# Kernel tuning notes

Hardware: AMD Instinct MI355X
Metric: run time of the kernel (lower is better)

The kernel has to match this reference:

```python
import jax, jax.numpy as jnp
import numpy as np

N_NODES = 50000
N_EDGES = 400000
DIM = 64
HEADS = 4
BN_EPS = 1e-5


def glorot(key, shape, fan_in, fan_out):
    std = np.sqrt(6.0 / (fan_in + fan_out))
    return jax.random.uniform(key, shape, jnp.float32, -std, std)


def setup_inputs() -> dict:
    key = jax.random.key(0)
    ks = jax.random.split(key, 6)
    x = jax.random.normal(ks[0], (N_NODES, DIM), jnp.float32)
    edge_attr = jax.random.normal(ks[1], (N_EDGES, DIM), jnp.float32)
    edge_index = jax.random.randint(ks[2], (2, N_EDGES), 0, N_NODES, jnp.int64)
    W = glorot(ks[3], (2 * DIM, HEADS * DIM), 2 * DIM, HEADS * DIM)
    att = glorot(ks[4], (1, HEADS, 2 * DIM), 2 * DIM, 1)
    bias = jnp.zeros((DIM,), jnp.float32)
    bn_gamma = jnp.ones((HEADS,), jnp.float32)
    bn_beta = jnp.zeros((HEADS,), jnp.float32)
    return {"x": x, "edge_attr": edge_attr, "W": W, "att": att,
            "bias": bias, "bn_gamma": bn_gamma, "bn_beta": bn_beta,
            "edge_index": edge_index}


def segment_softmax(a, seg, num_segments):
    # numerically stable softmax over variable-size neighborhoods (per segment)
    m = jax.ops.segment_max(a, seg, num_segments=num_segments)
    e = jnp.exp(a - m[seg])
    s = jax.ops.segment_sum(e, seg, num_segments=num_segments)
    return e / (s[seg] + 1e-16)


def reference(x, edge_attr, W, att, bias, bn_gamma, bn_beta, edge_index):
    act = jax.nn.softplus
    i, j = edge_index[0], edge_index[1]  # flow='target_to_source': i indexes x_i and aggregation
    x_i = x[i]                           # [E, D]
    x_j = x[j]                           # [E, D]
    out_i = act(jnp.concatenate([x_i, edge_attr], -1) @ W).reshape(-1, HEADS, DIM)
    out_j = act(jnp.concatenate([x_j, edge_attr], -1) @ W).reshape(-1, HEADS, DIM)
    # attention logits: [E, H]
    alpha = act((jnp.concatenate([out_i, out_j], -1) * att).sum(-1))
    # BatchNorm1d over heads with batch statistics (biased variance)
    mu = alpha.mean(0)
    var = alpha.var(0)
    alpha = (alpha - mu) * jax.lax.rsqrt(var + BN_EPS) * bn_gamma + bn_beta
    alpha = act(alpha)
    alpha = segment_softmax(alpha, i, N_NODES)     # softmax per target node
    msg = out_j * alpha[:, :, None]                # [E, H, D]
    aggr = jax.ops.segment_sum(msg, i, num_segments=N_NODES)  # [N, H, D]
    out = aggr.mean(1) + bias                      # mean over heads, then bias
    return out
```

## Files before the change

### kernel.cpp

```cpp
#include <hip/hip_runtime.h>
#include <hip/hip_bf16.h>

#define NN 50000
#define NE 400000
#define WTP 136

static const size_t OFF_ALPHA  = 0;
static const size_t OFF_SEGSUM = 6400000;
static const size_t OFF_BN     = 7200000;
static const size_t OFF_AGGR   = 7200256;
static const size_t OFF_IDX32  = 20000256;
static const size_t OFF_WT     = 23200256;
static const size_t OFF_XB     = 23265792;
static const size_t OFF_EAB    = 29665792;
static const size_t Z_SZ       = OFF_IDX32 - OFF_SEGSUM;

typedef __attribute__((ext_vector_type(8))) __bf16 bf16x8;
typedef __attribute__((ext_vector_type(4))) float  f32x4;
typedef __attribute__((ext_vector_type(4))) int    i32x4;
typedef __attribute__((ext_vector_type(2))) unsigned u32x2;

#define L2E 1.44269504f
#define LN2 0.69314718f

__device__ __forceinline__ float fexp2(float x) {
  float r; asm("v_exp_f32 %0, %1" : "=v"(r) : "v"(x)); return r;
}
__device__ __forceinline__ float flog2(float x) {
  float r; asm("v_log_f32 %0, %1" : "=v"(r) : "v"(x)); return r;
}
__device__ __forceinline__ float softplusf(float x) {
  return fmaxf(x, 0.0f) + LN2 * flog2(1.0f + fexp2(-L2E * fabsf(x)));
}
__device__ __forceinline__ float expsp(float y) {
  return fexp2(L2E * fmaxf(y, 0.0f)) * (1.0f + fexp2(-L2E * fabsf(y)));
}
__device__ __forceinline__ unsigned bfbits(float f) {
  return (unsigned)__builtin_bit_cast(unsigned short, __float2bfloat16(f));
}
__device__ __forceinline__ unsigned pkbf(float a, float b) {
  return bfbits(a) | (bfbits(b) << 16);
}
__device__ __forceinline__ bf16x8 ld8(const unsigned short* p) {
  return __builtin_bit_cast(bf16x8, *reinterpret_cast<const i32x4*>(p));
}
__device__ __forceinline__ bf16x8 ld8nt(const unsigned short* p) {
  i32x4 v = __builtin_nontemporal_load(reinterpret_cast<const i32x4*>(p));
  return __builtin_bit_cast(bf16x8, v);
}
__device__ __forceinline__ f32x4 ld4fnt(const float* p) {
  return __builtin_nontemporal_load(reinterpret_cast<const f32x4*>(p));
}
#define MFMA __builtin_amdgcn_mfma_f32_16x16x32_bf16

__global__ __launch_bounds__(256)
void k_idx_detect(const unsigned* __restrict__ src, unsigned* __restrict__ flag)
{
  int t = blockIdx.x * 256 + threadIdx.x;
  unsigned v = (t < NE) ? src[2 * t + 1] : 0u;
  if (__any(v != 0)) { if ((threadIdx.x & 63) == 0) atomicOr(flag, 1u); }
}
__global__ __launch_bounds__(256)
void k_idx_cvt(const unsigned* __restrict__ src, const unsigned* __restrict__ flag,
               int* __restrict__ dst)
{
  int e = blockIdx.x * 256 + threadIdx.x;
  unsigned f = *flag;
  dst[e] = (int)(f ? src[e] : src[2 * e]);
}

__global__ __launch_bounds__(256)
void k_wprep(const float* __restrict__ W, __hip_bfloat16* __restrict__ wt)
{
  int t = blockIdx.x * 256 + threadIdx.x;
  int k = t >> 8, c = t & 255;
  wt[c * 128 + k] = __float2bfloat16(W[t]);
}

__global__ __launch_bounds__(256)
void k_cvt_bf16(const float* __restrict__ src, unsigned* __restrict__ dst)
{
  int t = blockIdx.x * 256 + threadIdx.x;
  f32x4 v = *reinterpret_cast<const f32x4*>(src + (size_t)t * 4);
  u32x2 p = { pkbf(v[0], v[1]), pkbf(v[2], v[3]) };
  *reinterpret_cast<u32x2*>(dst + (size_t)t * 2) = p;
}

__device__ __forceinline__ void stage_wt(unsigned short* wtl,
                                         const unsigned short* wtu, int tid)
{
  for (int it = tid; it < 4096; it += 512) {
    int c = it >> 4, k8 = (it & 15) << 3;
    *reinterpret_cast<i32x4*>(&wtl[c * WTP + k8]) =
        *reinterpret_cast<const i32x4*>(wtu + c * 128 + k8);
  }
}

__global__ __launch_bounds__(512, 2)
void k_edge_alpha(const __hip_bfloat16* __restrict__ xb,
                  const __hip_bfloat16* __restrict__ eab,
                  const __hip_bfloat16* __restrict__ wt,
                  const float* __restrict__ att, const int* __restrict__ idx,
                  float* __restrict__ alpha, float* __restrict__ bnst)
{
  __shared__ __align__(16) unsigned short wtl[256 * WTP];
  __shared__ float attl[512];
  __shared__ float red[64];
  const unsigned short* wtu = reinterpret_cast<const unsigned short*>(wt);
  stage_wt(wtl, wtu, threadIdx.x);
  if (threadIdx.x < 512) attl[threadIdx.x] = att[threadIdx.x];
  __syncthreads();

  const int wave = threadIdx.x >> 6, lane = threadIdx.x & 63;
  const int m = lane & 15, rg = lane >> 4;
  const unsigned short* xbu = reinterpret_cast<const unsigned short*>(xb);
  const unsigned short* eau = reinterpret_cast<const unsigned short*>(eab);
  const int e0r = blockIdx.x * 256 + wave * 32;
  const bool oob = (e0r >= NE);
  const int e0 = oob ? 0 : e0r;

  const int iA = idx[e0 + m],      jA = idx[NE + e0 + m];
  const int iB = idx[e0 + 16 + m], jB = idx[NE + e0 + 16 + m];
  bf16x8 xiA0 = ld8(xbu + (size_t)iA * 64 + rg * 8);
  bf16x8 xiA1 = ld8(xbu + (size_t)iA * 64 + 32 + rg * 8);
  bf16x8 xjA0 = ld8(xbu + (size_t)jA * 64 + rg * 8);
  bf16x8 xjA1 = ld8(xbu + (size_t)jA * 64 + 32 + rg * 8);
  bf16x8 eA0  = ld8nt(eau + (size_t)(e0 + m) * 64 + rg * 8);
  bf16x8 eA1  = ld8nt(eau + (size_t)(e0 + m) * 64 + 32 + rg * 8);
  bf16x8 xiB0 = ld8(xbu + (size_t)iB * 64 + rg * 8);
  bf16x8 xiB1 = ld8(xbu + (size_t)iB * 64 + 32 + rg * 8);
  bf16x8 xjB0 = ld8(xbu + (size_t)jB * 64 + rg * 8);
  bf16x8 xjB1 = ld8(xbu + (size_t)jB * 64 + 32 + rg * 8);
  bf16x8 eB0  = ld8nt(eau + (size_t)(e0 + 16 + m) * 64 + rg * 8);
  bf16x8 eB1  = ld8nt(eau + (size_t)(e0 + 16 + m) * 64 + 32 + rg * 8);

  f32x4 pA0 = {0.f,0.f,0.f,0.f}, pA1 = pA0, pA2 = pA0, pA3 = pA0;
  f32x4 pB0 = pA0, pB1 = pA0, pB2 = pA0, pB3 = pA0;

#pragma unroll
  for (int t = 0; t < 16; ++t) {
    const unsigned short* wp = wtl + (t * 16 + m) * WTP + rg * 8;
    bf16x8 bx0 = ld8(wp);
    bf16x8 bx1 = ld8(wp + 32);
    bf16x8 be0 = ld8(wp + 64);
    bf16x8 be1 = ld8(wp + 96);
    f32x4 ciA = {0.f,0.f,0.f,0.f};
    ciA = MFMA(xiA0, bx0, ciA, 0, 0, 0);
    ciA = MFMA(xiA1, bx1, ciA, 0, 0, 0);
    ciA = MFMA(eA0,  be0, ciA, 0, 0, 0);
    ciA = MFMA(eA1,  be1, ciA, 0, 0, 0);
    f32x4 cjA = {0.f,0.f,0.f,0.f};
    cjA = MFMA(xjA0, bx0, cjA, 0, 0, 0);
    cjA = MFMA(xjA1, bx1, cjA, 0, 0, 0);
    cjA = MFMA(eA0,  be0, cjA, 0, 0, 0);
    cjA = MFMA(eA1,  be1, cjA, 0, 0, 0);
    f32x4 ciB = {0.f,0.f,0.f,0.f};
    ciB = MFMA(xiB0, bx0, ciB, 0, 0, 0);
    ciB = MFMA(xiB1, bx1, ciB, 0, 0, 0);
    ciB = MFMA(eB0,  be0, ciB, 0, 0, 0);
    ciB = MFMA(eB1,  be1, ciB, 0, 0, 0);
    f32x4 cjB = {0.f,0.f,0.f,0.f};
    cjB = MFMA(xjB0, bx0, cjB, 0, 0, 0);
    cjB = MFMA(xjB1, bx1, cjB, 0, 0, 0);
    cjB = MFMA(eB0,  be0, cjB, 0, 0, 0);
    cjB = MFMA(eB1,  be1, cjB, 0, 0, 0);
    const int h = t >> 2;
    const float ai = attl[h * 128 + (t & 3) * 16 + m];
    const float aj = attl[h * 128 + 64 + (t & 3) * 16 + m];
    pA0[h] = fmaf(softplusf(ciA[0]), ai, fmaf(softplusf(cjA[0]), aj, pA0[h]));
    pA1[h] = fmaf(softplusf(ciA[1]), ai, fmaf(softplusf(cjA[1]), aj, pA1[h]));
    pA2[h] = fmaf(softplusf(ciA[2]), ai, fmaf(softplusf(cjA[2]), aj, pA2[h]));
    pA3[h] = fmaf(softplusf(ciA[3]), ai, fmaf(softplusf(cjA[3]), aj, pA3[h]));
    pB0[h] = fmaf(softplusf(ciB[0]), ai, fmaf(softplusf(cjB[0]), aj, pB0[h]));
    pB1[h] = fmaf(softplusf(ciB[1]), ai, fmaf(softplusf(cjB[1]), aj, pB1[h]));
    pB2[h] = fmaf(softplusf(ciB[2]), ai, fmaf(softplusf(cjB[2]), aj, pB2[h]));
    pB3[h] = fmaf(softplusf(ciB[3]), ai, fmaf(softplusf(cjB[3]), aj, pB3[h]));
  }

  float bs = 0.f, ss = 0.f;
#pragma unroll
  for (int h = 0; h < 4; ++h) {
    pA0[h] += __shfl_xor(pA0[h], 1); pA0[h] += __shfl_xor(pA0[h], 2);
    pA0[h] += __shfl_xor(pA0[h], 4); pA0[h] += __shfl_xor(pA0[h], 8);
    pA1[h] += __shfl_xor(pA1[h], 1); pA1[h] += __shfl_xor(pA1[h], 2);
    pA1[h] += __shfl_xor(pA1[h], 4); pA1[h] += __shfl_xor(pA1[h], 8);
    pA2[h] += __shfl_xor(pA2[h], 1); pA2[h] += __shfl_xor(pA2[h], 2);
    pA2[h] += __shfl_xor(pA2[h], 4); pA2[h] += __shfl_xor(pA2[h], 8);
    pA3[h] += __shfl_xor(pA3[h], 1); pA3[h] += __shfl_xor(pA3[h], 2);
    pA3[h] += __shfl_xor(pA3[h], 4); pA3[h] += __shfl_xor(pA3[h], 8);
    pB0[h] += __shfl_xor(pB0[h], 1); pB0[h] += __shfl_xor(pB0[h], 2);
    pB0[h] += __shfl_xor(pB0[h], 4); pB0[h] += __shfl_xor(pB0[h], 8);
    pB1[h] += __shfl_xor(pB1[h], 1); pB1[h] += __shfl_xor(pB1[h], 2);
    pB1[h] += __shfl_xor(pB1[h], 4); pB1[h] += __shfl_xor(pB1[h], 8);
    pB2[h] += __shfl_xor(pB2[h], 1); pB2[h] += __shfl_xor(pB2[h], 2);
    pB2[h] += __shfl_xor(pB2[h], 4); pB2[h] += __shfl_xor(pB2[h], 8);
    pB3[h] += __shfl_xor(pB3[h], 1); pB3[h] += __shfl_xor(pB3[h], 2);
    pB3[h] += __shfl_xor(pB3[h], 4); pB3[h] += __shfl_xor(pB3[h], 8);
  }
  if (m < 4) {
    float vA0 = (m == 0) ? pA0[0] : (m == 1) ? pA0[1] : (m == 2) ? pA0[2] : pA0[3];
    float vA1 = (m == 0) ? pA1[0] : (m == 1) ? pA1[1] : (m == 2) ? pA1[2] : pA1[3];
    float vA2 = (m == 0) ? pA2[0] : (m == 1) ? pA2[1] : (m == 2) ? pA2[2] : pA2[3];
    float vA3 = (m == 0) ? pA3[0] : (m == 1) ? pA3[1] : (m == 2) ? pA3[2] : pA3[3];
    float vB0 = (m == 0) ? pB0[0] : (m == 1) ? pB0[1] : (m == 2) ? pB0[2] : pB0[3];
    float vB1 = (m == 0) ? pB1[0] : (m == 1) ? pB1[1] : (m == 2) ? pB1[2] : pB1[3];
    float vB2 = (m == 0) ? pB2[0] : (m == 1) ? pB2[1] : (m == 2) ? pB2[2] : pB2[3];
    float vB3 = (m == 0) ? pB3[0] : (m == 1) ? pB3[1] : (m == 2) ? pB3[2] : pB3[3];
    vA0 = softplusf(vA0); vA1 = softplusf(vA1); vA2 = softplusf(vA2); vA3 = softplusf(vA3);
    vB0 = softplusf(vB0); vB1 = softplusf(vB1); vB2 = softplusf(vB2); vB3 = softplusf(vB3);
    if (!oob) {
      alpha[(size_t)(e0 + rg * 4 + 0) * 4 + m] = vA0;
      alpha[(size_t)(e0 + rg * 4 + 1) * 4 + m] = vA1;
      alpha[(size_t)(e0 + rg * 4 + 2) * 4 + m] = vA2;
      alpha[(size_t)(e0 + rg * 4 + 3) * 4 + m] = vA3;
      alpha[(size_t)(e0 + 16 + rg * 4 + 0) * 4 + m] = vB0;
      alpha[(size_t)(e0 + 16 + rg * 4 + 1) * 4 + m] = vB1;
      alpha[(size_t)(e0 + 16 + rg * 4 + 2) * 4 + m] = vB2;
      alpha[(size_t)(e0 + 16 + rg * 4 + 3) * 4 + m] = vB3;
      bs = vA0 + vA1 + vA2 + vA3 + vB0 + vB1 + vB2 + vB3;
      ss = vA0*vA0 + vA1*vA1 + vA2*vA2 + vA3*vA3 + vB0*vB0 + vB1*vB1 + vB2*vB2 + vB3*vB3;
    }
  }
  bs += __shfl_xor(bs, 16); bs += __shfl_xor(bs, 32);
  ss += __shfl_xor(ss, 16); ss += __shfl_xor(ss, 32);
  if (lane < 4) { red[wave * 8 + lane] = bs; red[wave * 8 + 4 + lane] = ss; }
  __syncthreads();
  if (threadIdx.x < 8) {
    float s = 0.f;
#pragma unroll
    for (int w2 = 0; w2 < 8; ++w2) s += red[w2 * 8 + threadIdx.x];
    atomicAdd(&bnst[threadIdx.x], s);
  }
}

__global__ void k_bn_fin(float* __restrict__ bnst, const float* __restrict__ gamma)
{
  int q = threadIdx.x;
  if (q < 4) {
    float mu = bnst[q] * (1.0f / NE);
    float var = bnst[4 + q] * (1.0f / NE) - mu * mu;
    bnst[8 + q] = mu;
    bnst[12 + q] = rsqrtf(var + 1e-5f) * gamma[q];
  }
}

__global__ __launch_bounds__(256)
void k_bn_expsum(float* __restrict__ alpha, const int* __restrict__ idx,
                 const float* __restrict__ bnst, const float* __restrict__ beta,
                 float* __restrict__ segsum)
{
  int e = blockIdx.x * 256 + threadIdx.x;
  if (e >= NE) return;
  float4 a = *reinterpret_cast<const float4*>(&alpha[(size_t)e * 4]);
  int n = idx[e];
  a.x = expsp((a.x - bnst[8])  * bnst[12] + beta[0]);
  a.y = expsp((a.y - bnst[9])  * bnst[13] + beta[1]);
  a.z = expsp((a.z - bnst[10]) * bnst[14] + beta[2]);
  a.w = expsp((a.w - bnst[11]) * bnst[15] + beta[3]);
  *reinterpret_cast<float4*>(&alpha[(size_t)e * 4]) = a;
  atomicAdd(&segsum[n * 4 + 0], a.x);
  atomicAdd(&segsum[n * 4 + 1], a.y);
  atomicAdd(&segsum[n * 4 + 2], a.z);
  atomicAdd(&segsum[n * 4 + 3], a.w);
}

__global__ __launch_bounds__(256, 3)
void k_edge_aggr(const __hip_bfloat16* __restrict__ xb,
                 const __hip_bfloat16* __restrict__ eab,
                 const __hip_bfloat16* __restrict__ wt,
                 const int* __restrict__ idx, const float* __restrict__ alpha,
                 const float* __restrict__ segsum, float* __restrict__ aggr)
{
  const int wave = threadIdx.x >> 6, lane = threadIdx.x & 63;
  const int m = lane & 15, rg = lane >> 4;
  const unsigned short* xbu = reinterpret_cast<const unsigned short*>(xb);
  const unsigned short* eau = reinterpret_cast<const unsigned short*>(eab);
  const unsigned short* wtu = reinterpret_cast<const unsigned short*>(wt);
  const int e0 = blockIdx.x * 128 + wave * 32;

  const int jA = idx[NE + e0 + m], jB = idx[NE + e0 + 16 + m];
  bf16x8 xjA0 = ld8(xbu + (size_t)jA * 64 + rg * 8);
  bf16x8 xjA1 = ld8(xbu + (size_t)jA * 64 + 32 + rg * 8);
  bf16x8 eA0  = ld8nt(eau + (size_t)(e0 + m) * 64 + rg * 8);
  bf16x8 eA1  = ld8nt(eau + (size_t)(e0 + m) * 64 + 32 + rg * 8);
  bf16x8 xjB0 = ld8(xbu + (size_t)jB * 64 + rg * 8);
  bf16x8 xjB1 = ld8(xbu + (size_t)jB * 64 + 32 + rg * 8);
  bf16x8 eB0  = ld8nt(eau + (size_t)(e0 + 16 + m) * 64 + rg * 8);
  bf16x8 eB1  = ld8nt(eau + (size_t)(e0 + 16 + m) * 64 + 32 + rg * 8);

  const int iA0 = idx[e0 + rg * 4 + 0];
  const int iA1 = idx[e0 + rg * 4 + 1];
  const int iA2 = idx[e0 + rg * 4 + 2];
  const int iA3 = idx[e0 + rg * 4 + 3];
  const int iB0 = idx[e0 + 16 + rg * 4 + 0];
  const int iB1 = idx[e0 + 16 + rg * 4 + 1];
  const int iB2 = idx[e0 + 16 + rg * 4 + 2];
  const int iB3 = idx[e0 + 16 + rg * 4 + 3];

  f32x4 wA0, wA1, wA2, wA3, wB0, wB1, wB2, wB3;
  {
    f32x4 ev0 = ld4fnt(alpha + (size_t)(e0 + rg * 4 + 0) * 4);
    f32x4 ev1 = ld4fnt(alpha + (size_t)(e0 + rg * 4 + 1) * 4);
    f32x4 ev2 = ld4fnt(alpha + (size_t)(e0 + rg * 4 + 2) * 4);
    f32x4 ev3 = ld4fnt(alpha + (size_t)(e0 + rg * 4 + 3) * 4);
    f32x4 fv0 = ld4fnt(alpha + (size_t)(e0 + 16 + rg * 4 + 0) * 4);
    f32x4 fv1 = ld4fnt(alpha + (size_t)(e0 + 16 + rg * 4 + 1) * 4);
    f32x4 fv2 = ld4fnt(alpha + (size_t)(e0 + 16 + rg * 4 + 2) * 4);
    f32x4 fv3 = ld4fnt(alpha + (size_t)(e0 + 16 + rg * 4 + 3) * 4);
    f32x4 sA0 = *reinterpret_cast<const f32x4*>(segsum + (size_t)iA0 * 4);
    f32x4 sA1 = *reinterpret_cast<const f32x4*>(segsum + (size_t)iA1 * 4);
    f32x4 sA2 = *reinterpret_cast<const f32x4*>(segsum + (size_t)iA2 * 4);
    f32x4 sA3 = *reinterpret_cast<const f32x4*>(segsum + (size_t)iA3 * 4);
    f32x4 sB0 = *reinterpret_cast<const f32x4*>(segsum + (size_t)iB0 * 4);
    f32x4 sB1 = *reinterpret_cast<const f32x4*>(segsum + (size_t)iB1 * 4);
    f32x4 sB2 = *reinterpret_cast<const f32x4*>(segsum + (size_t)iB2 * 4);
    f32x4 sB3 = *reinterpret_cast<const f32x4*>(segsum + (size_t)iB3 * 4);
#pragma unroll
    for (int h = 0; h < 4; ++h) {
      wA0[h] = 0.25f * ev0[h] / (sA0[h] + 1e-16f);
      wA1[h] = 0.25f * ev1[h] / (sA1[h] + 1e-16f);
      wA2[h] = 0.25f * ev2[h] / (sA2[h] + 1e-16f);
      wA3[h] = 0.25f * ev3[h] / (sA3[h] + 1e-16f);
      wB0[h] = 0.25f * fv0[h] / (sB0[h] + 1e-16f);
      wB1[h] = 0.25f * fv1[h] / (sB1[h] + 1e-16f);
      wB2[h] = 0.25f * fv2[h] / (sB2[h] + 1e-16f);
      wB3[h] = 0.25f * fv3[h] / (sB3[h] + 1e-16f);
    }
  }

  f32x4 cA0 = {0.f,0.f,0.f,0.f}, cA1 = cA0, cA2 = cA0, cA3 = cA0;
  f32x4 cB0 = cA0, cB1 = cA0, cB2 = cA0, cB3 = cA0;

#pragma unroll
  for (int t = 0; t < 16; ++t) {
    const unsigned short* wp = wtu + (t * 16 + m) * 128 + rg * 8;
    bf16x8 bx0 = ld8(wp);
    bf16x8 bx1 = ld8(wp + 32);
    bf16x8 be0 = ld8(wp + 64);
    bf16x8 be1 = ld8(wp + 96);
    f32x4 cjA = {0.f,0.f,0.f,0.f};
    cjA = MFMA(xjA0, bx0, cjA, 0, 0, 0);
    cjA = MFMA(xjA1, bx1, cjA, 0, 0, 0);
    cjA = MFMA(eA0,  be0, cjA, 0, 0, 0);
    cjA = MFMA(eA1,  be1, cjA, 0, 0, 0);
    f32x4 cjB = {0.f,0.f,0.f,0.f};
    cjB = MFMA(xjB0, bx0, cjB, 0, 0, 0);
    cjB = MFMA(xjB1, bx1, cjB, 0, 0, 0);
    cjB = MFMA(eB0,  be0, cjB, 0, 0, 0);
    cjB = MFMA(eB1,  be1, cjB, 0, 0, 0);
    const int h = t >> 2, tq = t & 3;
    cA0[tq] = fmaf(softplusf(cjA[0]), wA0[h], cA0[tq]);
    cA1[tq] = fmaf(softplusf(cjA[1]), wA1[h], cA1[tq]);
    cA2[tq] = fmaf(softplusf(cjA[2]), wA2[h], cA2[tq]);
    cA3[tq] = fmaf(softplusf(cjA[3]), wA3[h], cA3[tq]);
    cB0[tq] = fmaf(softplusf(cjB[0]), wB0[h], cB0[tq]);
    cB1[tq] = fmaf(softplusf(cjB[1]), wB1[h], cB1[tq]);
    cB2[tq] = fmaf(softplusf(cjB[2]), wB2[h], cB2[tq]);
    cB3[tq] = fmaf(softplusf(cjB[3]), wB3[h], cB3[tq]);
  }

#pragma unroll
  for (int tq = 0; tq < 4; ++tq) {
    atomicAdd(&aggr[(size_t)iA0 * 64 + tq * 16 + m], cA0[tq]);
    atomicAdd(&aggr[(size_t)iA1 * 64 + tq * 16 + m], cA1[tq]);
    atomicAdd(&aggr[(size_t)iA2 * 64 + tq * 16 + m], cA2[tq]);
    atomicAdd(&aggr[(size_t)iA3 * 64 + tq * 16 + m], cA3[tq]);
    atomicAdd(&aggr[(size_t)iB0 * 64 + tq * 16 + m], cB0[tq]);
    atomicAdd(&aggr[(size_t)iB1 * 64 + tq * 16 + m], cB1[tq]);
    atomicAdd(&aggr[(size_t)iB2 * 64 + tq * 16 + m], cB2[tq]);
    atomicAdd(&aggr[(size_t)iB3 * 64 + tq * 16 + m], cB3[tq]);
  }
}

__global__ __launch_bounds__(256)
void k_final(const float* __restrict__ aggr, const float* __restrict__ bias,
             float* __restrict__ out)
{
  int t = blockIdx.x * 256 + threadIdx.x;
  out[t] = aggr[t] + bias[t & 63];
}

extern "C" void kernel_launch(void* const* d_in, const int* in_sizes, int n_in,
                              void* d_out, int out_size, void* d_ws, size_t ws_size,
                              hipStream_t stream)
{
  const float* x    = (const float*)d_in[0];
  const float* ea   = (const float*)d_in[1];
  const float* W    = (const float*)d_in[2];
  const float* att  = (const float*)d_in[3];
  const float* bias = (const float*)d_in[4];
  const float* gam  = (const float*)d_in[5];
  const float* bet  = (const float*)d_in[6];
  const unsigned* idx_raw = (const unsigned*)d_in[7];
  float* out = (float*)d_out;

  char* ws = (char*)d_ws;
  float*    alpha  = (float*)(ws + OFF_ALPHA);
  float*    segsum = (float*)(ws + OFF_SEGSUM);
  float*    bnst   = (float*)(ws + OFF_BN);
  unsigned* flag   = (unsigned*)(ws + OFF_BN + 64);
  float*    aggr   = (float*)(ws + OFF_AGGR);
  int*      idx    = (int*)(ws + OFF_IDX32);
  __hip_bfloat16* wt  = (__hip_bfloat16*)(ws + OFF_WT);
  __hip_bfloat16* xb  = (__hip_bfloat16*)(ws + OFF_XB);
  __hip_bfloat16* eab = (__hip_bfloat16*)(ws + OFF_EAB);

  hipMemsetAsync(ws + OFF_SEGSUM, 0, Z_SZ, stream);
  k_wprep<<<128, 256, 0, stream>>>(W, wt);
  k_idx_detect<<<(NE + 255) / 256, 256, 0, stream>>>(idx_raw, flag);
  k_idx_cvt<<<(2 * NE) / 256, 256, 0, stream>>>(idx_raw, flag, idx);
  k_cvt_bf16<<<(NN * 64 / 4) / 256, 256, 0, stream>>>(x, (unsigned*)xb);
  k_cvt_bf16<<<(NE * 64 / 4) / 256, 256, 0, stream>>>(ea, (unsigned*)eab);

  const int NB512 = (NE + 255) / 256;
  k_edge_alpha<<<NB512, 512, 0, stream>>>(xb, eab, wt, att, idx, alpha, bnst);
  k_bn_fin<<<1, 64, 0, stream>>>(bnst, gam);
  k_bn_expsum<<<(NE + 255) / 256, 256, 0, stream>>>(alpha, idx, bnst, bet, segsum);
  k_edge_aggr<<<NE / 128, 256, 0, stream>>>(xb, eab, wt, idx, alpha, segsum, aggr);
  k_final<<<(NN * 64) / 256, 256, 0, stream>>>(aggr, bias, out);
}
```

Measured before the change: 446.5 us.

## Counting-sort edges by target and merge same-target atomics in aggregation

Builds a per-call counting sort of edges by target node: a histogram, a two-level scan and an atomic scatter into a permutation. The aggregation kernel then walks edges in sorted order and merges consecutive contributions to the same target in registers before issuing atomics. The goal is fewer global float atomics. In exchange it adds four extra kernels and a memset, and the edge_attr, alpha and index reads in aggregation become gathers rather than contiguous loads. With about 8 edges per node, each 4-edge group merges to roughly one or two targets.

```diff
diff --git a/kernel.cpp b/kernel.cpp
--- a/kernel.cpp
+++ b/kernel.cpp
@@ -13,7 +13,14 @@
 static const size_t OFF_WT     = 23200256;
 static const size_t OFF_XB     = 23265792;
 static const size_t OFF_EAB    = 29665792;
+static const size_t OFF_CNT    = 80865792;
+static const size_t OFF_CUR    = 81066496;
+static const size_t OFF_PART   = 81267200;
+static const size_t OFF_BSUM   = 81467904;
+static const size_t OFF_BOFS   = 81468928;
+static const size_t OFF_SRT    = 81469952;
 static const size_t Z_SZ       = OFF_IDX32 - OFF_SEGSUM;
+static const size_t ZC_SZ      = 401408;
 
 typedef __attribute__((ext_vector_type(8))) __bf16 bf16x8;
 typedef __attribute__((ext_vector_type(4))) float  f32x4;
@@ -67,6 +74,53 @@
   int e = blockIdx.x * 256 + threadIdx.x;
   unsigned f = *flag;
   dst[e] = (int)(f ? src[e] : src[2 * e]);
+}
+
+__global__ __launch_bounds__(256)
+void k_hist(const int* __restrict__ idx, int* __restrict__ cnt)
+{
+  int e = blockIdx.x * 256 + threadIdx.x;
+  if (e < NE) atomicAdd(&cnt[idx[e]], 1);
+}
+__global__ __launch_bounds__(256)
+void k_scan1(const int* __restrict__ cnt, int* __restrict__ part, int* __restrict__ bsum)
+{
+  __shared__ int s[256];
+  int g = blockIdx.x * 256 + threadIdx.x;
+  int v = (g < NN) ? cnt[g] : 0;
+  s[threadIdx.x] = v; __syncthreads();
+  for (int off = 1; off < 256; off <<= 1) {
+    int t = (threadIdx.x >= off) ? s[threadIdx.x - off] : 0;
+    __syncthreads();
+    s[threadIdx.x] += t;
+    __syncthreads();
+  }
+  part[g] = s[threadIdx.x] - v;
+  if (threadIdx.x == 255) bsum[blockIdx.x] = s[255];
+}
+__global__ void k_scan2(const int* __restrict__ bsum, int* __restrict__ bofs)
+{
+  __shared__ int s[256];
+  int v = (threadIdx.x < 196) ? bsum[threadIdx.x] : 0;
+  s[threadIdx.x] = v; __syncthreads();
+  for (int off = 1; off < 256; off <<= 1) {
+    int t = (threadIdx.x >= off) ? s[threadIdx.x - off] : 0;
+    __syncthreads();
+    s[threadIdx.x] += t;
+    __syncthreads();
+  }
+  bofs[threadIdx.x] = s[threadIdx.x] - v;
+}
+__global__ __launch_bounds__(256)
+void k_scatter(const int* __restrict__ idx, const int* __restrict__ part,
+               const int* __restrict__ bofs, int* __restrict__ cur,
+               int* __restrict__ srt)
+{
+  int e = blockIdx.x * 256 + threadIdx.x;
+  if (e >= NE) return;
+  int n = idx[e];
+  int p = part[n] + bofs[n >> 8] + atomicAdd(&cur[n], 1);
+  srt[p] = e;
 }
 
 __global__ __launch_bounds__(256)
@@ -264,11 +318,20 @@
   atomicAdd(&segsum[n * 4 + 3], a.w);
 }
 
+__device__ __forceinline__ void flush4(float* __restrict__ aggr, int tgt, f32x4 a, int m)
+{
+  atomicAdd(&aggr[(size_t)tgt * 64 +      m], a[0]);
+  atomicAdd(&aggr[(size_t)tgt * 64 + 16 + m], a[1]);
+  atomicAdd(&aggr[(size_t)tgt * 64 + 32 + m], a[2]);
+  atomicAdd(&aggr[(size_t)tgt * 64 + 48 + m], a[3]);
+}
+
 __global__ __launch_bounds__(256, 3)
 void k_edge_aggr(const __hip_bfloat16* __restrict__ xb,
                  const __hip_bfloat16* __restrict__ eab,
                  const __hip_bfloat16* __restrict__ wt,
-                 const int* __restrict__ idx, const float* __restrict__ alpha,
+                 const int* __restrict__ idx, const int* __restrict__ srt,
+                 const float* __restrict__ alpha,
                  const float* __restrict__ segsum, float* __restrict__ aggr)
 {
   const int wave = threadIdx.x >> 6, lane = threadIdx.x & 63;
@@ -276,37 +339,36 @@
   const unsigned short* xbu = reinterpret_cast<const unsigned short*>(xb);
   const unsigned short* eau = reinterpret_cast<const unsigned short*>(eab);
   const unsigned short* wtu = reinterpret_cast<const unsigned short*>(wt);
-  const int e0 = blockIdx.x * 128 + wave * 32;
-
-  const int jA = idx[NE + e0 + m], jB = idx[NE + e0 + 16 + m];
+  const int k0 = blockIdx.x * 128 + wave * 32;
+
+  const int eAm = srt[k0 + m], eBm = srt[k0 + 16 + m];
+  const int jA = idx[NE + eAm], jB = idx[NE + eBm];
   bf16x8 xjA0 = ld8(xbu + (size_t)jA * 64 + rg * 8);
   bf16x8 xjA1 = ld8(xbu + (size_t)jA * 64 + 32 + rg * 8);
-  bf16x8 eA0  = ld8nt(eau + (size_t)(e0 + m) * 64 + rg * 8);
-  bf16x8 eA1  = ld8nt(eau + (size_t)(e0 + m) * 64 + 32 + rg * 8);
+  bf16x8 eA0  = ld8nt(eau + (size_t)eAm * 64 + rg * 8);
+  bf16x8 eA1  = ld8nt(eau + (size_t)eAm * 64 + 32 + rg * 8);
   bf16x8 xjB0 = ld8(xbu + (size_t)jB * 64 + rg * 8);
   bf16x8 xjB1 = ld8(xbu + (size_t)jB * 64 + 32 + rg * 8);
-  bf16x8 eB0  = ld8nt(eau + (size_t)(e0 + 16 + m) * 64 + rg * 8);
-  bf16x8 eB1  = ld8nt(eau + (size_t)(e0 + 16 + m) * 64 + 32 + rg * 8);
-
-  const int iA0 = idx[e0 + rg * 4 + 0];
-  const int iA1 = idx[e0 + rg * 4 + 1];
-  const int iA2 = idx[e0 + rg * 4 + 2];
-  const int iA3 = idx[e0 + rg * 4 + 3];
-  const int iB0 = idx[e0 + 16 + rg * 4 + 0];
-  const int iB1 = idx[e0 + 16 + rg * 4 + 1];
-  const int iB2 = idx[e0 + 16 + rg * 4 + 2];
-  const int iB3 = idx[e0 + 16 + rg * 4 + 3];
+  bf16x8 eB0  = ld8nt(eau + (size_t)eBm * 64 + rg * 8);
+  bf16x8 eB1  = ld8nt(eau + (size_t)eBm * 64 + 32 + rg * 8);
+
+  const int eqA0 = srt[k0 + rg * 4 + 0], eqA1 = srt[k0 + rg * 4 + 1];
+  const int eqA2 = srt[k0 + rg * 4 + 2], eqA3 = srt[k0 + rg * 4 + 3];
+  const int eqB0 = srt[k0 + 16 + rg * 4 + 0], eqB1 = srt[k0 + 16 + rg * 4 + 1];
+  const int eqB2 = srt[k0 + 16 + rg * 4 + 2], eqB3 = srt[k0 + 16 + rg * 4 + 3];
+  const int iA0 = idx[eqA0], iA1 = idx[eqA1], iA2 = idx[eqA2], iA3 = idx[eqA3];
+  const int iB0 = idx[eqB0], iB1 = idx[eqB1], iB2 = idx[eqB2], iB3 = idx[eqB3];
 
   f32x4 wA0, wA1, wA2, wA3, wB0, wB1, wB2, wB3;
   {
-    f32x4 ev0 = ld4fnt(alpha + (size_t)(e0 + rg * 4 + 0) * 4);
-    f32x4 ev1 = ld4fnt(alpha + (size_t)(e0 + rg * 4 + 1) * 4);
-    f32x4 ev2 = ld4fnt(alpha + (size_t)(e0 + rg * 4 + 2) * 4);
-    f32x4 ev3 = ld4fnt(alpha + (size_t)(e0 + rg * 4 + 3) * 4);
-    f32x4 fv0 = ld4fnt(alpha + (size_t)(e0 + 16 + rg * 4 + 0) * 4);
-    f32x4 fv1 = ld4fnt(alpha + (size_t)(e0 + 16 + rg * 4 + 1) * 4);
-    f32x4 fv2 = ld4fnt(alpha + (size_t)(e0 + 16 + rg * 4 + 2) * 4);
-    f32x4 fv3 = ld4fnt(alpha + (size_t)(e0 + 16 + rg * 4 + 3) * 4);
+    f32x4 ev0 = ld4fnt(alpha + (size_t)eqA0 * 4);
+    f32x4 ev1 = ld4fnt(alpha + (size_t)eqA1 * 4);
+    f32x4 ev2 = ld4fnt(alpha + (size_t)eqA2 * 4);
+    f32x4 ev3 = ld4fnt(alpha + (size_t)eqA3 * 4);
+    f32x4 fv0 = ld4fnt(alpha + (size_t)eqB0 * 4);
+    f32x4 fv1 = ld4fnt(alpha + (size_t)eqB1 * 4);
+    f32x4 fv2 = ld4fnt(alpha + (size_t)eqB2 * 4);
+    f32x4 fv3 = ld4fnt(alpha + (size_t)eqB3 * 4);
     f32x4 sA0 = *reinterpret_cast<const f32x4*>(segsum + (size_t)iA0 * 4);
     f32x4 sA1 = *reinterpret_cast<const f32x4*>(segsum + (size_t)iA1 * 4);
     f32x4 sA2 = *reinterpret_cast<const f32x4*>(segsum + (size_t)iA2 * 4);
@@ -359,16 +421,19 @@
     cB3[tq] = fmaf(softplusf(cjB[3]), wB3[h], cB3[tq]);
   }
 
-#pragma unroll
-  for (int tq = 0; tq < 4; ++tq) {
-    atomicAdd(&aggr[(size_t)iA0 * 64 + tq * 16 + m], cA0[tq]);
-    atomicAdd(&aggr[(size_t)iA1 * 64 + tq * 16 + m], cA1[tq]);
-    atomicAdd(&aggr[(size_t)iA2 * 64 + tq * 16 + m], cA2[tq]);
-    atomicAdd(&aggr[(size_t)iA3 * 64 + tq * 16 + m], cA3[tq]);
-    atomicAdd(&aggr[(size_t)iB0 * 64 + tq * 16 + m], cB0[tq]);
-    atomicAdd(&aggr[(size_t)iB1 * 64 + tq * 16 + m], cB1[tq]);
-    atomicAdd(&aggr[(size_t)iB2 * 64 + tq * 16 + m], cB2[tq]);
-    atomicAdd(&aggr[(size_t)iB3 * 64 + tq * 16 + m], cB3[tq]);
+  {
+    f32x4 acc = cA0; int tgt = iA0;
+    if (iA1 == tgt) acc += cA1; else { flush4(aggr, tgt, acc, m); tgt = iA1; acc = cA1; }
+    if (iA2 == tgt) acc += cA2; else { flush4(aggr, tgt, acc, m); tgt = iA2; acc = cA2; }
+    if (iA3 == tgt) acc += cA3; else { flush4(aggr, tgt, acc, m); tgt = iA3; acc = cA3; }
+    flush4(aggr, tgt, acc, m);
+  }
+  {
+    f32x4 acc = cB0; int tgt = iB0;
+    if (iB1 == tgt) acc += cB1; else { flush4(aggr, tgt, acc, m); tgt = iB1; acc = cB1; }
+    if (iB2 == tgt) acc += cB2; else { flush4(aggr, tgt, acc, m); tgt = iB2; acc = cB2; }
+    if (iB3 == tgt) acc += cB3; else { flush4(aggr, tgt, acc, m); tgt = iB3; acc = cB3; }
+    flush4(aggr, tgt, acc, m);
   }
 }
 
@@ -404,18 +469,30 @@
   __hip_bfloat16* wt  = (__hip_bfloat16*)(ws + OFF_WT);
   __hip_bfloat16* xb  = (__hip_bfloat16*)(ws + OFF_XB);
   __hip_bfloat16* eab = (__hip_bfloat16*)(ws + OFF_EAB);
+  int* cnt  = (int*)(ws + OFF_CNT);
+  int* cur  = (int*)(ws + OFF_CUR);
+  int* part = (int*)(ws + OFF_PART);
+  int* bsum = (int*)(ws + OFF_BSUM);
+  int* bofs = (int*)(ws + OFF_BOFS);
+  int* srt  = (int*)(ws + OFF_SRT);
 
   hipMemsetAsync(ws + OFF_SEGSUM, 0, Z_SZ, stream);
+  hipMemsetAsync(ws + OFF_CNT, 0, ZC_SZ, stream);
   k_wprep<<<128, 256, 0, stream>>>(W, wt);
   k_idx_detect<<<(NE + 255) / 256, 256, 0, stream>>>(idx_raw, flag);
   k_idx_cvt<<<(2 * NE) / 256, 256, 0, stream>>>(idx_raw, flag, idx);
   k_cvt_bf16<<<(NN * 64 / 4) / 256, 256, 0, stream>>>(x, (unsigned*)xb);
   k_cvt_bf16<<<(NE * 64 / 4) / 256, 256, 0, stream>>>(ea, (unsigned*)eab);
 
+  k_hist<<<(NE + 255) / 256, 256, 0, stream>>>(idx, cnt);
+  k_scan1<<<196, 256, 0, stream>>>(cnt, part, bsum);
+  k_scan2<<<1, 256, 0, stream>>>(bsum, bofs);
+  k_scatter<<<(NE + 255) / 256, 256, 0, stream>>>(idx, part, bofs, cur, srt);
+
   const int NB512 = (NE + 255) / 256;
   k_edge_alpha<<<NB512, 512, 0, stream>>>(xb, eab, wt, att, idx, alpha, bnst);
   k_bn_fin<<<1, 64, 0, stream>>>(bnst, gam);
   k_bn_expsum<<<(NE + 255) / 256, 256, 0, stream>>>(alpha, idx, bnst, bet, segsum);
-  k_edge_aggr<<<NE / 128, 256, 0, stream>>>(xb, eab, wt, idx, alpha, segsum, aggr);
+  k_edge_aggr<<<NE / 128, 256, 0, stream>>>(xb, eab, wt, idx, srt, alpha, segsum, aggr);
   k_final<<<(NN * 64) / 256, 256, 0, stream>>>(aggr, bias, out);
 }
```

After: 792.5 us. 1.77x slower.
